# Optimization experiments

Measured on AMD Instinct MI355X. Metric: run time of the kernel, lower is better.

## Reference

```python
import jax, jax.numpy as jnp
import numpy as np

N = 50000      # query points
N0 = 50000     # support points
M = 32         # neighbors per query
K = 15         # kernel points
DIM = 3
D_IN = 64
D_OUT = 64
POINT_INFLUENCE = 1.0
KERNEL_RADIUS = 1.5 * POINT_INFLUENCE  # _INFLUENCE_TO_RADIUS * point_influence


def setup_inputs() -> dict:
    key = jax.random.key(0)
    k1, k2, k3, k4, k5 = jax.random.split(key, 5)
    query_points = jax.random.normal(k1, (N, DIM), jnp.float32)
    support_points = jax.random.normal(k2, (N0, DIM), jnp.float32)
    neighbors = jax.random.randint(k3, (N, M), 0, N0 + 1)  # index N0 = shadow point
    x = jax.random.normal(k4, (N0, D_IN), jnp.float32)
    # Kernel point dispositions: fixed center point, rest spread within kernel radius
    # (stand-in for kernel_point_optimization_debug; K_points is a frozen parameter).
    rng = np.random.RandomState(0)
    kp = rng.uniform(-1.0, 1.0, (K, DIM))
    kp[0, :] = 0.0
    kp = kp * (KERNEL_RADIUS / np.max(np.linalg.norm(kp, axis=1)))
    K_points = jnp.asarray(kp, dtype=jnp.float32)
    # Xavier-normal conv weights [K, D_IN, D_OUT]
    std = (2.0 / (D_IN + D_OUT)) ** 0.5
    weight = jax.random.normal(k5, (K, D_IN, D_OUT), jnp.float32) * std
    return {
        "query_points": query_points,
        "support_points": support_points,
        "neighbors": neighbors,
        "x": x,
        "K_points": K_points,
        "weight": weight,
    }


def reference(query_points, support_points, neighbors, x, K_points, weight):
    # Shadow support point far away + zero shadow feature row
    shadow = jnp.full((1, query_points.shape[1]), 1e6, dtype=support_points.dtype)
    sp = jnp.concatenate([support_points, shadow], axis=0)            # [N0+1, 3]
    xp = jnp.concatenate([x, jnp.zeros((1, x.shape[1]), x.dtype)], axis=0)  # [N0+1, d]

    # Gather neighbor coords, center on query point
    neighb_pts = sp[neighbors] - query_points[:, None, :]             # [N, M, 3]
    # Squared distances to each kernel point
    diff = neighb_pts[:, :, None, :] - K_points[None, None, :, :]     # [N, M, K, 3]
    sq_distances = jnp.sum(diff * diff, axis=-1)                      # [N, M, K]

    # Linear influence, then transpose to [N, K, M]
    all_weights = jnp.clip(1.0 - jnp.sqrt(sq_distances) / POINT_INFLUENCE, 0.0)
    all_weights = jnp.swapaxes(all_weights, 1, 2)                     # [N, K, M]

    # Gather neighbor features and aggregate per kernel point
    feats = xp[neighbors]                                             # [N, M, d]
    weighted = jnp.einsum("nkm,nmd->nkd", all_weights, feats)        # [N, K, d]
    # Apply per-kernel-point weight matrices and sum over kernel points
    out = jnp.einsum("nkd,kdo->no", weighted, weight)                # [N, out]
    return out
```

## Files before the change

kernel.cpp:

```cpp
#include <hip/hip_runtime.h>

#define NQ 50000
#define NS 50000
#define MNB 32
#define KP 15
#define DF 64
#define WTS 968
#define WQS 40

typedef __bf16 bf16x8 __attribute__((ext_vector_type(8)));
typedef float  f32x4  __attribute__((ext_vector_type(4)));

__device__ __forceinline__ unsigned short bf1(float f) {
    union { __bf16 h; unsigned short s; } r; r.h = (__bf16)f; return r.s;
}
__device__ __forceinline__ unsigned pk2(float a, float b) {
    union { __bf16 h[2]; unsigned u; } r;
    r.h[0] = (__bf16)a; r.h[1] = (__bf16)b; return r.u;
}

__global__ __launch_bounds__(256) void preconv(
    const float* __restrict__ x, const float* __restrict__ W,
    unsigned short* __restrict__ xbp, uint4* __restrict__ wBf)
{
    const int b = blockIdx.x;
    if (b < NS / 16) {
        const int row = b * 16 + (threadIdx.x >> 4);
        const int cl  = threadIdx.x & 15;
        const float f0 = x[row * DF + 0 * 16 + cl];
        const float f1 = x[row * DF + 1 * 16 + cl];
        const float f2 = x[row * DF + 2 * 16 + cl];
        const float f3 = x[row * DF + 3 * 16 + cl];
        uint2 o; o.x = pk2(f0, f1); o.y = pk2(f2, f3);
        *(uint2*)&xbp[row * DF + cl * 4] = o;
    } else {
        const int chunk = (b - NS / 16) * 256 + threadIdx.x;
        if (chunk >= 7680) return;
        const int tc = chunk >> 6, c = chunk & 63;
        union { unsigned short s[8]; uint4 u; } pk;
        #pragma unroll
        for (int j = 0; j < 8; ++j) {
            const int kappa = tc * 8 + j;
            const int k  = kappa >> 6;
            const int cb = kappa & 3;
            const int t  = (kappa >> 2) & 15;
            pk.s[j] = bf1(W[(size_t)(k * 64 + cb * 16 + t) * 64 + c]);
        }
        wBf[chunk] = pk.u;
    }
}

__global__ __launch_bounds__(1024, 8) void kpconv_fused(
    const float* __restrict__ qp, const float* __restrict__ sp,
    const int* __restrict__ nb, const uint2* __restrict__ xb2,
    const float* __restrict__ kpts, const uint4* __restrict__ wBf,
    float* __restrict__ out)
{
    __shared__ struct {
        __align__(16) unsigned short wt[16 * WTS];
        __align__(16) unsigned short wq[16][16 * WQS];
        __align__(16) unsigned int   ids[16][MNB];
    } sm;

    const int tid  = threadIdx.x;
    const int lane = tid & 63, wv = tid >> 6;
    const int kh = lane >> 5, m = lane & 31;
    const int n0 = blockIdx.x * 16;
    const int n  = n0 + wv;

    const int id = nb[n * MNB + m];
    const float qx = qp[n * 3 + 0], qy = qp[n * 3 + 1], qz = qp[n * 3 + 2];
    float sx = 1e6f, sy = 1e6f, sz = 1e6f;
    if (id < NS) { sx = sp[id * 3 + 0]; sy = sp[id * 3 + 1]; sz = sp[id * 3 + 2]; }
    const float rx = sx - qx, ry = sy - qy, rz = sz - qz;
    #pragma unroll
    for (int j = 0; j < 8; ++j) {
        const int k = kh * 8 + j;
        const int kc = (k < KP) ? k : 0;
        const float dx = rx - kpts[kc * 3 + 0];
        const float dy = ry - kpts[kc * 3 + 1];
        const float dz = rz - kpts[kc * 3 + 2];
        const float wkj = fmaxf(1.0f - sqrtf(dx * dx + dy * dy + dz * dz), 0.0f);
        if (k < KP) sm.wq[wv][k * WQS + m] = bf1(wkj);
    }
    if (kh == 0) sm.ids[wv][m] = (id < NS) ? (unsigned)id : 0u;

    const int cl = lane & 15, q = lane >> 4;
    union { uint4 u; bf16x8 v; } af;
    af.u = *(const uint4*)&sm.wq[wv][cl * WQS + q * 8];
    const uint4 ia = *(const uint4*)&sm.ids[wv][q * 8];
    const uint4 ib = *(const uint4*)&sm.ids[wv][q * 8 + 4];
    const uint2 r0 = xb2[(size_t)ia.x * 16 + cl];
    const uint2 r1 = xb2[(size_t)ia.y * 16 + cl];
    const uint2 r2 = xb2[(size_t)ia.z * 16 + cl];
    const uint2 r3 = xb2[(size_t)ia.w * 16 + cl];
    const uint2 r4 = xb2[(size_t)ib.x * 16 + cl];
    const uint2 r5 = xb2[(size_t)ib.y * 16 + cl];
    const uint2 r6 = xb2[(size_t)ib.z * 16 + cl];
    const uint2 r7 = xb2[(size_t)ib.w * 16 + cl];
    #define PRM(hi, lo, sel) __builtin_amdgcn_perm((hi), (lo), (sel))
    const unsigned S0 = 0x05040100u, S1 = 0x07060302u;
    union { uint4 u; bf16x8 v; } bf[4];
    bf[0].u = (uint4){PRM(r1.x, r0.x, S0), PRM(r3.x, r2.x, S0), PRM(r5.x, r4.x, S0), PRM(r7.x, r6.x, S0)};
    bf[1].u = (uint4){PRM(r1.x, r0.x, S1), PRM(r3.x, r2.x, S1), PRM(r5.x, r4.x, S1), PRM(r7.x, r6.x, S1)};
    bf[2].u = (uint4){PRM(r1.y, r0.y, S0), PRM(r3.y, r2.y, S0), PRM(r5.y, r4.y, S0), PRM(r7.y, r6.y, S0)};
    bf[3].u = (uint4){PRM(r1.y, r0.y, S1), PRM(r3.y, r2.y, S1), PRM(r5.y, r4.y, S1), PRM(r7.y, r6.y, S1)};
    #undef PRM
    const f32x4 zero = (f32x4){0.f, 0.f, 0.f, 0.f};
    f32x4 acc1[4];
    #pragma unroll
    for (int cb = 0; cb < 4; ++cb)
        acc1[cb] = __builtin_amdgcn_mfma_f32_16x16x32_bf16(af.v, bf[cb].v, zero, 0, 0, 0);

    #pragma unroll
    for (int i = 0; i < 4; ++i) {
        const int k = q * 4 + i;
        if (k < KP) {
            uint2 pkd;
            pkd.x = pk2(acc1[0][i], acc1[1][i]);
            pkd.y = pk2(acc1[2][i], acc1[3][i]);
            *(uint2*)&sm.wt[wv * WTS + (k * 16 + cl) * 4] = pkd;
        }
    }
    __syncthreads();
    if (wv >= 4) return;

    f32x4 dacc = (f32x4){0.f, 0.f, 0.f, 0.f};
    #pragma unroll 6
    for (int ks = 0; ks < 30; ++ks) {
        const bf16x8 a = *(const bf16x8*)&sm.wt[cl * WTS + ks * 32 + q * 8];
        union { uint4 u; bf16x8 v; } bu;
        bu.u = wBf[(4 * ks + q) * 64 + wv * 16 + cl];
        dacc = __builtin_amdgcn_mfma_f32_16x16x32_bf16(a, bu.v, dacc, 0, 0, 0);
    }
    #pragma unroll
    for (int i = 0; i < 4; ++i)
        out[(size_t)(n0 + q * 4 + i) * 64 + wv * 16 + cl] = dacc[i];
}

extern "C" void kernel_launch(void* const* d_in, const int* in_sizes, int n_in,
                              void* d_out, int out_size, void* d_ws, size_t ws_size,
                              hipStream_t stream) {
    const float* qp   = (const float*)d_in[0];
    const float* sp   = (const float*)d_in[1];
    const int*   nb   = (const int*)d_in[2];
    const float* x    = (const float*)d_in[3];
    const float* kpts = (const float*)d_in[4];
    const float* W    = (const float*)d_in[5];
    float* out = (float*)d_out;

    uint4*          wBf = (uint4*)d_ws;
    unsigned short* xbp = (unsigned short*)((char*)d_ws + 122880);

    hipLaunchKernelGGL(preconv, dim3(NS / 16 + 30), dim3(256), 0, stream,
                       x, W, xbp, wBf);
    hipLaunchKernelGGL(kpconv_fused, dim3(NQ / 16), dim3(1024), 0, stream,
                       qp, sp, nb, (const uint2*)xbp, kpts, wBf, out);
}
```

Baseline: 129.3 us.

## Compact active neighbors via ballot and skip feature gathers for zero-weight neighbors

Each wave computes which neighbors have any nonzero kernel influence, uses a ballot and popcount to compact active neighbors to the front of the MFMA K dimension, and only gathers bf16 feature rows for groups containing active neighbors. Inactive slots point to a new zeroed padding row written by an extra preconv block. This removes random global gathers for far neighbors, at the cost of extra ballot/popcount work and a permuted shared-memory layout.

```diff
diff --git a/kernel.cpp b/kernel.cpp
--- a/kernel.cpp
+++ b/kernel.cpp
@@ -33,9 +33,8 @@
         const float f3 = x[row * DF + 3 * 16 + cl];
         uint2 o; o.x = pk2(f0, f1); o.y = pk2(f2, f3);
         *(uint2*)&xbp[row * DF + cl * 4] = o;
-    } else {
+    } else if (b < NS / 16 + 30) {
         const int chunk = (b - NS / 16) * 256 + threadIdx.x;
-        if (chunk >= 7680) return;
         const int tc = chunk >> 6, c = chunk & 63;
         union { unsigned short s[8]; uint4 u; } pk;
         #pragma unroll
@@ -47,6 +46,9 @@
             pk.s[j] = bf1(W[(size_t)(k * 64 + cb * 16 + t) * 64 + c]);
         }
         wBf[chunk] = pk.u;
+    } else {
+        if (threadIdx.x < 8)
+            ((uint4*)(xbp + (size_t)NS * DF))[threadIdx.x] = (uint4){0, 0, 0, 0};
     }
 }
 
@@ -73,6 +75,7 @@
     float sx = 1e6f, sy = 1e6f, sz = 1e6f;
     if (id < NS) { sx = sp[id * 3 + 0]; sy = sp[id * 3 + 1]; sz = sp[id * 3 + 2]; }
     const float rx = sx - qx, ry = sy - qy, rz = sz - qz;
+    float wk[8], wmax = 0.0f;
     #pragma unroll
     for (int j = 0; j < 8; ++j) {
         const int k = kh * 8 + j;
@@ -80,31 +83,43 @@
         const float dx = rx - kpts[kc * 3 + 0];
         const float dy = ry - kpts[kc * 3 + 1];
         const float dz = rz - kpts[kc * 3 + 2];
-        const float wkj = fmaxf(1.0f - sqrtf(dx * dx + dy * dy + dz * dz), 0.0f);
-        if (k < KP) sm.wq[wv][k * WQS + m] = bf1(wkj);
+        wk[j] = fmaxf(1.0f - sqrtf(dx * dx + dy * dy + dz * dz), 0.0f);
+        wmax = fmaxf(wmax, wk[j]);
     }
-    if (kh == 0) sm.ids[wv][m] = (id < NS) ? (unsigned)id : 0u;
+    const unsigned long long bal = __ballot(wmax > 0.0f);
+    const unsigned comb = (unsigned)(bal & 0xFFFFFFFFull) | (unsigned)(bal >> 32);
+    const int A = __popc(comb);
+    const bool act = (comb >> m) & 1u;
+    const unsigned mlow = (1u << m) - 1u;
+    const int p = act ? __popc(comb & mlow) : (A + __popc(~comb & mlow));
+    const int s = (p & 3) * 8 + (p >> 2);
+    #pragma unroll
+    for (int j = 0; j < 8; ++j) {
+        const int k = kh * 8 + j;
+        if (k < KP) sm.wq[wv][k * WQS + s] = bf1(wk[j]);
+    }
+    if (kh == 0) sm.ids[wv][p] = act ? (unsigned)id : (unsigned)NS;
 
     const int cl = lane & 15, q = lane >> 4;
     union { uint4 u; bf16x8 v; } af;
     af.u = *(const uint4*)&sm.wq[wv][cl * WQS + q * 8];
-    const uint4 ia = *(const uint4*)&sm.ids[wv][q * 8];
-    const uint4 ib = *(const uint4*)&sm.ids[wv][q * 8 + 4];
-    const uint2 r0 = xb2[(size_t)ia.x * 16 + cl];
-    const uint2 r1 = xb2[(size_t)ia.y * 16 + cl];
-    const uint2 r2 = xb2[(size_t)ia.z * 16 + cl];
-    const uint2 r3 = xb2[(size_t)ia.w * 16 + cl];
-    const uint2 r4 = xb2[(size_t)ib.x * 16 + cl];
-    const uint2 r5 = xb2[(size_t)ib.y * 16 + cl];
-    const uint2 r6 = xb2[(size_t)ib.z * 16 + cl];
-    const uint2 r7 = xb2[(size_t)ib.w * 16 + cl];
+    uint2 r[8];
+    #pragma unroll
+    for (int j = 0; j < 8; ++j) r[j] = (uint2){0u, 0u};
+    #pragma unroll
+    for (int j = 0; j < 8; ++j) {
+        if (4 * j < A) {
+            const unsigned sid = sm.ids[wv][4 * j + q];
+            r[j] = xb2[(size_t)sid * 16 + cl];
+        }
+    }
     #define PRM(hi, lo, sel) __builtin_amdgcn_perm((hi), (lo), (sel))
     const unsigned S0 = 0x05040100u, S1 = 0x07060302u;
     union { uint4 u; bf16x8 v; } bf[4];
-    bf[0].u = (uint4){PRM(r1.x, r0.x, S0), PRM(r3.x, r2.x, S0), PRM(r5.x, r4.x, S0), PRM(r7.x, r6.x, S0)};
-    bf[1].u = (uint4){PRM(r1.x, r0.x, S1), PRM(r3.x, r2.x, S1), PRM(r5.x, r4.x, S1), PRM(r7.x, r6.x, S1)};
-    bf[2].u = (uint4){PRM(r1.y, r0.y, S0), PRM(r3.y, r2.y, S0), PRM(r5.y, r4.y, S0), PRM(r7.y, r6.y, S0)};
-    bf[3].u = (uint4){PRM(r1.y, r0.y, S1), PRM(r3.y, r2.y, S1), PRM(r5.y, r4.y, S1), PRM(r7.y, r6.y, S1)};
+    bf[0].u = (uint4){PRM(r[1].x, r[0].x, S0), PRM(r[3].x, r[2].x, S0), PRM(r[5].x, r[4].x, S0), PRM(r[7].x, r[6].x, S0)};
+    bf[1].u = (uint4){PRM(r[1].x, r[0].x, S1), PRM(r[3].x, r[2].x, S1), PRM(r[5].x, r[4].x, S1), PRM(r[7].x, r[6].x, S1)};
+    bf[2].u = (uint4){PRM(r[1].y, r[0].y, S0), PRM(r[3].y, r[2].y, S0), PRM(r[5].y, r[4].y, S0), PRM(r[7].y, r[6].y, S0)};
+    bf[3].u = (uint4){PRM(r[1].y, r[0].y, S1), PRM(r[3].y, r[2].y, S1), PRM(r[5].y, r[4].y, S1), PRM(r[7].y, r[6].y, S1)};
     #undef PRM
     const f32x4 zero = (f32x4){0.f, 0.f, 0.f, 0.f};
     f32x4 acc1[4];
@@ -152,7 +167,7 @@
     uint4*          wBf = (uint4*)d_ws;
     unsigned short* xbp = (unsigned short*)((char*)d_ws + 122880);
 
-    hipLaunchKernelGGL(preconv, dim3(NS / 16 + 30), dim3(256), 0, stream,
+    hipLaunchKernelGGL(preconv, dim3(NS / 16 + 31), dim3(256), 0, stream,
                        x, W, xbp, wBf);
     hipLaunchKernelGGL(kpconv_fused, dim3(NQ / 16), dim3(1024), 0, stream,
                        qp, sp, nb, (const uint2*)xbp, kpts, wBf, out);
```

New measurement: 126.5 us. 1.02x faster.
